# Kernel tuning notes

Measured on AMD Instinct MI355X. Metric: run time of the kernel, lower is better.

The kernel has to match this reference:

```python
import jax, jax.numpy as jnp
import numpy as np

LMAX, MMAX = 6, 2
CIN = COUT = 128
NUM_EDGES = 50000
NUM_M_COMP = (LMAX + 1) + sum(2 * (LMAX + 1 - m) for m in range(1, MMAX + 1))  # 29


def setup_inputs() -> dict:
    key = jax.random.key(0)
    ks = jax.random.split(key, 4)
    x = jax.random.normal(ks[0], (NUM_EDGES, NUM_M_COMP, CIN), dtype=jnp.float32)
    d0 = (LMAX + 1) * CIN  # 896
    W0 = jax.random.normal(ks[1], (d0, d0), dtype=jnp.float32) / np.float32(np.sqrt(d0))
    b0 = jnp.zeros((d0,), dtype=jnp.float32)
    Ws = []
    for i, m in enumerate(range(1, MMAX + 1)):
        din = (LMAX + 1 - m) * CIN
        dout = (LMAX + 1 - m) * COUT
        # torch Linear init then mul_(1/sqrt(2)); random scaled init suffices for a baseline
        Ws.append(jax.random.normal(ks[2 + i], (2 * dout, din), dtype=jnp.float32)
                  / np.float32(np.sqrt(2.0) * np.sqrt(din)))
    return {"x": x, "W0": W0, "b0": b0, "W1": Ws[0], "W2": Ws[1]}


def reference(x, W0, b0, W1, W2):
    E = x.shape[0]
    Wm = [W1, W2]
    outs = []
    # m = 0 block: flatten (lmax+1, Cin) -> single Linear with bias
    x0 = x[:, :LMAX + 1].reshape(E, (LMAX + 1) * CIN)
    y0 = x0 @ W0.T + b0                               # [E, (lmax+1)*Cout]
    outs.append(y0.reshape(E, LMAX + 1, COUT))
    offset = LMAX + 1
    for m in range(1, MMAX + 1):
        n = LMAX + 1 - m
        xm = x[:, offset:offset + 2 * n].reshape(E, 2, n * CIN)  # [E, 2(real/imag), n*Cin]
        offset += 2 * n
        ym = jnp.einsum('eti,oi->eto', xm, Wm[m - 1])            # [E, 2, 2*n*Cout]
        of = n * COUT
        x_r, x_i = ym[..., :of], ym[..., of:]
        pos = x_r[:, 0] - x_i[:, 1]                              # [E, n*Cout]
        neg = x_r[:, 1] + x_i[:, 0]
        outs.append(pos.reshape(E, n, COUT))
        outs.append(neg.reshape(E, n, COUT))
    return jnp.concatenate(outs, axis=1)  # [E, num_m_components, Cout]
```

## Files before the change

kernel.cpp:

```cpp
#include <hip/hip_runtime.h>
#include <hip/hip_bf16.h>
#include <cstdint>
#include <cstddef>

typedef __bf16 bf16_t;
typedef __bf16 bf16x8 __attribute__((ext_vector_type(8)));
typedef __bf16 bf16x4 __attribute__((ext_vector_type(4)));
typedef float f32x4 __attribute__((ext_vector_type(4)));

static constexpr int LD = 29 * 128;


__global__ void cvt_w0_pad_kernel(const float* __restrict__ in, bf16_t* __restrict__ out,
                                  int rows_real, int kdim, int total) {
    int idx = blockIdx.x * 256 + threadIdx.x;
    if (idx >= total) return;
    int r = idx / kdim;
    int c = idx - r * kdim;
    out[idx] = (bf16_t)((r < rows_real) ? in[(size_t)r * kdim + c] : 0.f);
}

__global__ void combine_wm_kernel(const float* __restrict__ W, bf16_t* __restrict__ Wc,
                                  int of, int din, int total) {
    int idx = blockIdx.x * 256 + threadIdx.x;
    if (idx >= total) return;
    int twodin = 2 * din;
    int r = idx / twodin;
    int c = idx - r * twodin;
    float v;
    if (r < of) {
        v = (c < din) ? W[(size_t)r * din + c]
                      : -W[(size_t)(r + of) * din + (c - din)];
    } else {
        int j = r - of;
        v = (c < din) ? W[(size_t)(j + of) * din + c]
                      : W[(size_t)j * din + (c - din)];
    }
    Wc[idx] = (bf16_t)v;
}

__global__ void cvt_x_kernel(const float* __restrict__ in, bf16_t* __restrict__ out, long n8) {
    long stride = (long)gridDim.x * 256;
    for (long i = blockIdx.x * 256L + threadIdx.x; i < n8; i += stride) {
        f32x4 v0 = *(const f32x4*)(in + i * 8);
        f32x4 v1 = *(const f32x4*)(in + i * 8 + 4);
        bf16x8 h;
        h[0] = (bf16_t)v0[0]; h[1] = (bf16_t)v0[1];
        h[2] = (bf16_t)v0[2]; h[3] = (bf16_t)v0[3];
        h[4] = (bf16_t)v1[0]; h[5] = (bf16_t)v1[1];
        h[6] = (bf16_t)v1[2]; h[7] = (bf16_t)v1[3];
        *(bf16x8*)(out + i * 8) = h;
    }
}


#define MMA_Q(QM, QN, AF)                                                            \
    do {                                                                             \
        __builtin_amdgcn_s_setprio(1);                                               \
        _Pragma("unroll") for (int i_ = 0; i_ < 2; ++i_)                             \
        _Pragma("unroll") for (int j_ = 0; j_ < 4; ++j_)                             \
        _Pragma("unroll") for (int kk_ = 0; kk_ < 2; ++kk_)                          \
            acc[QM][QN][i_][j_] = __builtin_amdgcn_mfma_f32_16x16x32_bf16(           \
                AF[i_][kk_], b[j_][kk_], acc[QM][QN][i_][j_], 0, 0, 0);              \
        __builtin_amdgcn_s_setprio(0);                                               \
    } while (0)

#define BAR() __builtin_amdgcn_s_barrier()
#define LGKM0()                                                   \
    do {                                                          \
        asm volatile("s_waitcnt lgkmcnt(0)" ::: "memory");        \
        __builtin_amdgcn_sched_barrier(0);                        \
    } while (0)

template <int NPAD, int K, int NREAL, bool BIAS>
__global__ __launch_bounds__(512, 2)
void gemm256_kernel(const bf16_t* __restrict__ Xb, const bf16_t* __restrict__ W,
                    const float* __restrict__ bias, float* __restrict__ Y, int M) {
    constexpr int NT  = K / 64;
    constexpr int NIT = NT / 2;
    static_assert(NT % 2 == 0, "NT must be even");

    __shared__ bf16_t lds[2][2][2][128][64];

    const int tid  = threadIdx.x;
    const int wid  = tid >> 6;
    const int lane = tid & 63;
    const int awr  = wid & 3;
    const int bwc  = wid >> 2;
    const int lrow = lane & 15;
    const int koff = lane >> 4;

    const long m0 = (long)blockIdx.y * 256;
    const long n0 = (long)blockIdx.x * 256;

    const int sr = tid >> 3;
    const int sc = tid & 7;

    auto stage_half = [&](int bu, int op, int half, int kt) {
        #pragma unroll
        for (int s = 0; s < 2; ++s) {
            const int r  = s * 64 + sr;
            const int kc = sc ^ (r & 7);
            long grow = (op ? n0 : m0) + half * 128 + r;
            if (!op && grow >= M) grow = M - 1;
            const bf16_t* gsrc = (op ? W : Xb) + grow * (op ? (long)K : (long)LD) + kt * 64 + kc * 8;
            bf16_t* dst = &lds[bu][op][half][0][0] + s * 4096 + wid * 512;
            __builtin_amdgcn_global_load_lds(
                (const __attribute__((address_space(1))) void*)gsrc,
                (__attribute__((address_space(3))) void*)dst, 16, 0, 0);
        }
    };

    bf16x8 a0[2][2], a1[2][2], b[4][2];
    f32x4 acc[2][2][2][4] = {};

    auto load_a = [&](bf16x8 (&a)[2][2], int bu, int half) {
        #pragma unroll
        for (int i = 0; i < 2; ++i)
            #pragma unroll
            for (int kk = 0; kk < 2; ++kk) {
                const int rr = awr * 32 + i * 16 + lrow;
                const int sw = (kk * 4 + koff) ^ (rr & 7);
                a[i][kk] = *(const bf16x8*)(&lds[bu][0][half][rr][sw * 8]);
            }
    };
    auto load_b = [&](int bu, int half) {
        #pragma unroll
        for (int j = 0; j < 4; ++j)
            #pragma unroll
            for (int kk = 0; kk < 2; ++kk) {
                const int rr = bwc * 64 + j * 16 + lrow;
                const int sw = (kk * 4 + koff) ^ (rr & 7);
                b[j][kk] = *(const bf16x8*)(&lds[bu][1][half][rr][sw * 8]);
            }
    };

    auto half_iter = [&](int bu, int ts, bool do_stage, bool lastvm) {
        load_a(a0, bu, 0);
        load_b(bu, 0);
        BAR(); LGKM0();
        MMA_Q(0, 0, a0);
        BAR();
        load_a(a1, bu, 1);
        if (do_stage) { stage_half(bu, 0, 0, ts); stage_half(bu, 1, 0, ts); }
        BAR(); LGKM0();
        MMA_Q(1, 0, a1);
        BAR();
        load_b(bu, 1);
        if (do_stage) stage_half(bu, 0, 1, ts);
        BAR(); LGKM0();
        MMA_Q(1, 1, a1);
        BAR();
        if (do_stage) stage_half(bu, 1, 1, ts);
        if (lastvm) asm volatile("s_waitcnt vmcnt(0)" ::: "memory");
        else        asm volatile("s_waitcnt vmcnt(8)" ::: "memory");
        BAR(); LGKM0();
        MMA_Q(0, 1, a0);
        BAR();
    };

    #pragma unroll
    for (int h = 0; h < 2; ++h) { stage_half(0, 0, h, 0); stage_half(0, 1, h, 0); }
    #pragma unroll
    for (int h = 0; h < 2; ++h) { stage_half(1, 0, h, 1); stage_half(1, 1, h, 1); }
    asm volatile("s_waitcnt vmcnt(8)" ::: "memory");
    BAR();

    #pragma unroll 1
    for (int it = 0; it < NIT; ++it) {
        const bool st = (it < NIT - 1);
        const bool lv = (it == NIT - 1);
        half_iter(0, 2 * it + 2, st, lv);
        half_iter(1, 2 * it + 3, st, lv);
    }

    #pragma unroll
    for (int qm = 0; qm < 2; ++qm)
        #pragma unroll
        for (int qn = 0; qn < 2; ++qn)
            #pragma unroll
            for (int j = 0; j < 4; ++j) {
                const long col = n0 + qn * 128 + bwc * 64 + j * 16 + lrow;
                if (col < NREAL) {
                    float bv = 0.f;
                    if constexpr (BIAS) bv = bias[col];
                    #pragma unroll
                    for (int i = 0; i < 2; ++i) {
                        const long rbase = m0 + qm * 128 + awr * 32 + i * 16 + koff * 4;
                        #pragma unroll
                        for (int r = 0; r < 4; ++r) {
                            const long row = rbase + r;
                            if (row < M) Y[row * LD + col] = acc[qm][qn][i][j][r] + bv;
                        }
                    }
                }
            }
}


template <int N, int K, bool BIAS>
__global__ __launch_bounds__(256)
void gemm_fb_kernel(const float* __restrict__ X, const bf16_t* __restrict__ W,
                    const float* __restrict__ bias, float* __restrict__ Y, int M) {
    constexpr int BM = 128, BK = 32;
    constexpr int KT = K / BK;
    __shared__ bf16_t As[BM][BK + 8];
    __shared__ bf16_t Bs[BM][BK];
    const int tid = threadIdx.x, wid = tid >> 6, lane = tid & 63;
    const int wr = wid >> 1, wc = wid & 1;
    const int m0 = blockIdx.y * BM, n0 = blockIdx.x * 128;
    const int srow0 = wid * 16 + (lane >> 2), schunk = lane & 3;
    const int ar = tid >> 3, ac = (tid & 7) * 4;
    const int lrow = lane & 15, koff = lane >> 4;
    f32x4 acc[4][4] = {};
    for (int kt = 0; kt < KT; ++kt) {
        const int k0 = kt * BK;
        #pragma unroll
        for (int s = 0; s < 2; ++s) {
            const int row = srow0 + s * 64;
            const int kc = schunk ^ ((row >> 1) & 3);
            const bf16_t* gsrc = W + (size_t)(n0 + row) * K + k0 + kc * 8;
            bf16_t* ldsbase = &Bs[wid * 16 + s * 64][0];
            __builtin_amdgcn_global_load_lds(
                (const __attribute__((address_space(1))) void*)gsrc,
                (__attribute__((address_space(3))) void*)ldsbase, 16, 0, 0);
        }
        #pragma unroll
        for (int p = 0; p < 4; ++p) {
            const int row = p * 32 + ar;
            const int gr = m0 + row;
            f32x4 v = {};
            if (gr < M) v = *(const f32x4*)(X + (size_t)gr * LD + k0 + ac);
            bf16x4 h;
            h[0] = (bf16_t)v[0]; h[1] = (bf16_t)v[1];
            h[2] = (bf16_t)v[2]; h[3] = (bf16_t)v[3];
            *(bf16x4*)(&As[row][ac]) = h;
        }
        __syncthreads();
        bf16x8 a[4], bb[4];
        #pragma unroll
        for (int i = 0; i < 4; ++i) {
            a[i] = *(const bf16x8*)(&As[wr * 64 + i * 16 + lrow][koff * 8]);
            const int col = wc * 64 + i * 16 + lrow;
            const int kc = koff ^ ((col >> 1) & 3);
            bb[i] = *(const bf16x8*)(&Bs[col][kc * 8]);
        }
        #pragma unroll
        for (int i = 0; i < 4; ++i)
            #pragma unroll
            for (int j = 0; j < 4; ++j)
                acc[i][j] = __builtin_amdgcn_mfma_f32_16x16x32_bf16(a[i], bb[j], acc[i][j], 0, 0, 0);
        __syncthreads();
    }
    #pragma unroll
    for (int j = 0; j < 4; ++j) {
        const int col = n0 + wc * 64 + j * 16 + lrow;
        float bv = 0.f;
        if constexpr (BIAS) bv = bias[col];
        #pragma unroll
        for (int i = 0; i < 4; ++i) {
            const int rbase = m0 + wr * 64 + i * 16 + koff * 4;
            #pragma unroll
            for (int r = 0; r < 4; ++r) {
                const int gr = rbase + r;
                if (gr < M) Y[(size_t)gr * LD + col] = acc[i][j][r] + bv;
            }
        }
    }
}


extern "C" void kernel_launch(void* const* d_in, const int* in_sizes, int n_in,
                              void* d_out, int out_size, void* d_ws, size_t ws_size,
                              hipStream_t stream) {
    const float* x  = (const float*)d_in[0];
    const float* W0 = (const float*)d_in[1];
    const float* b0 = (const float*)d_in[2];
    const float* W1 = (const float*)d_in[3];
    const float* W2 = (const float*)d_in[4];
    float* out = (float*)d_out;

    const int E = in_sizes[0] / LD;

    constexpr size_t W0P = (size_t)1024 * 896;
    constexpr size_t W1S = (size_t)1536 * 1536;
    constexpr size_t W2S = (size_t)1280 * 1280;
    bf16_t* wc0 = (bf16_t*)d_ws;
    bf16_t* wc1 = wc0 + W0P;
    bf16_t* wc2 = wc1 + W1S;
    bf16_t* xb  = wc2 + W2S;

    const size_t need = (W0P + W1S + W2S + (size_t)E * LD) * sizeof(bf16_t);
    const bool fast = ws_size >= need;

    cvt_w0_pad_kernel<<<(int)((W0P + 255) / 256), 256, 0, stream>>>(W0, wc0, 896, 896, (int)W0P);
    combine_wm_kernel<<<(int)(W1S / 256), 256, 0, stream>>>(W1, wc1, 768, 768, (int)W1S);
    combine_wm_kernel<<<(int)(W2S / 256), 256, 0, stream>>>(W2, wc2, 640, 640, (int)W2S);

    if (fast) {
        const long n8 = (long)E * LD / 8;
        cvt_x_kernel<<<4096, 256, 0, stream>>>(x, xb, n8);
        const int mt = (E + 255) / 256;
        gemm256_kernel<1024, 896, 896, true>
            <<<dim3(4, mt), 512, 0, stream>>>(xb, wc0, b0, out, E);
        gemm256_kernel<1536, 1536, 1536, false>
            <<<dim3(6, mt), 512, 0, stream>>>(xb + 896, wc1, nullptr, out + 896, E);
        gemm256_kernel<1280, 1280, 1280, false>
            <<<dim3(5, mt), 512, 0, stream>>>(xb + 2432, wc2, nullptr, out + 2432, E);
    } else {
        const int mt = (E + 127) / 128;
        gemm_fb_kernel<896, 896, true>
            <<<dim3(896 / 128, mt), 256, 0, stream>>>(x, wc0, b0, out, E);
        gemm_fb_kernel<1536, 1536, false>
            <<<dim3(1536 / 128, mt), 256, 0, stream>>>(x + 896, wc1, nullptr, out + 896, E);
        gemm_fb_kernel<1280, 1280, false>
            <<<dim3(1280 / 128, mt), 256, 0, stream>>>(x + 2432, wc2, nullptr, out + 2432, E);
    }
}
```

Measured before the change: 864.0 us.

## Merge three GEMMs into one persistent kernel with cross-tile prefetch

Replaces the three separate templated GEMM launches with a single persistent kernel of 256 blocks. Each block walks a flat tile list covering all three m-blocks, using a runtime tile descriptor. The first k-slices of the next tile are staged while the current tile finishes, so the pipeline does not drain between tiles. This removes launch gaps and per-launch tail effects. In exchange K and NT become runtime values (fewer compile-time constants), the epilogue uses a runtime bias check, and tiles with different K are mixed in one static round-robin schedule that may balance poorly.

```diff
diff --git a/kernel.cpp b/kernel.cpp
--- a/kernel.cpp
+++ b/kernel.cpp
@@ -54,6 +54,17 @@
 }
 
 
+struct TileDesc {
+    const bf16_t* A;
+    const bf16_t* W;
+    float* Y;
+    const float* bias;
+    long m0;
+    int K;
+    int NT;
+    int ncol;
+};
+
 #define MMA_Q(QM, QN, AF)                                                            \
     do {                                                                             \
         __builtin_amdgcn_s_setprio(1);                                               \
@@ -72,14 +83,14 @@
         __builtin_amdgcn_sched_barrier(0);                        \
     } while (0)
 
-template <int NPAD, int K, int NREAL, bool BIAS>
 __global__ __launch_bounds__(512, 2)
-void gemm256_kernel(const bf16_t* __restrict__ Xb, const bf16_t* __restrict__ W,
-                    const float* __restrict__ bias, float* __restrict__ Y, int M) {
-    constexpr int NT  = K / 64;
-    constexpr int NIT = NT / 2;
-    static_assert(NT % 2 == 0, "NT must be even");
-
+void gemm_persist_kernel(const bf16_t* __restrict__ xb,
+                         const bf16_t* __restrict__ w0,
+                         const bf16_t* __restrict__ w1,
+                         const bf16_t* __restrict__ w2,
+                         const float* __restrict__ b0,
+                         float* __restrict__ out,
+                         int E, int mt, int ntiles) {
     __shared__ bf16_t lds[2][2][2][128][64];
 
     const int tid  = threadIdx.x;
@@ -89,21 +100,49 @@
     const int bwc  = wid >> 2;
     const int lrow = lane & 15;
     const int koff = lane >> 4;
-
-    const long m0 = (long)blockIdx.y * 256;
-    const long n0 = (long)blockIdx.x * 256;
-
-    const int sr = tid >> 3;
-    const int sc = tid & 7;
-
-    auto stage_half = [&](int bu, int op, int half, int kt) {
+    const int sr   = tid >> 3;
+    const int sc   = tid & 7;
+    const int P    = gridDim.x;
+
+    int t = blockIdx.x;
+    if (t >= ntiles) return;
+
+    auto make_desc = [&](int tt, TileDesc& d) {
+        const int S0 = 4 * mt, S1 = S0 + 6 * mt;
+        int mi, ni;
+        if (tt < S0) {
+            mi = tt >> 2; ni = tt & 3;
+            d.A = xb; d.W = w0 + (size_t)ni * 256 * 896;
+            d.Y = out + ni * 256; d.bias = b0 + ni * 256;
+            d.K = 896; d.NT = 14;
+            d.ncol = (896 - ni * 256 < 256) ? (896 - ni * 256) : 256;
+        } else if (tt < S1) {
+            int l = tt - S0; mi = l / 6; ni = l - mi * 6;
+            d.A = xb + 896; d.W = w1 + (size_t)ni * 256 * 1536;
+            d.Y = out + 896 + ni * 256; d.bias = nullptr;
+            d.K = 1536; d.NT = 24; d.ncol = 256;
+        } else {
+            int l = tt - S1; mi = l / 5; ni = l - mi * 5;
+            d.A = xb + 2432; d.W = w2 + (size_t)ni * 256 * 1280;
+            d.Y = out + 2432 + ni * 256; d.bias = nullptr;
+            d.K = 1280; d.NT = 20; d.ncol = 256;
+        }
+        d.m0 = (long)mi * 256;
+    };
+
+    auto stage_half = [&](const TileDesc& d, int kt, int bu, int op, int half) {
         #pragma unroll
         for (int s = 0; s < 2; ++s) {
             const int r  = s * 64 + sr;
             const int kc = sc ^ (r & 7);
-            long grow = (op ? n0 : m0) + half * 128 + r;
-            if (!op && grow >= M) grow = M - 1;
-            const bf16_t* gsrc = (op ? W : Xb) + grow * (op ? (long)K : (long)LD) + kt * 64 + kc * 8;
+            const bf16_t* gsrc;
+            if (op) {
+                gsrc = d.W + (size_t)(half * 128 + r) * d.K + kt * 64 + kc * 8;
+            } else {
+                long grow = d.m0 + half * 128 + r;
+                if (grow >= E) grow = E - 1;
+                gsrc = d.A + grow * (long)LD + kt * 64 + kc * 8;
+            }
             bf16_t* dst = &lds[bu][op][half][0][0] + s * 4096 + wid * 512;
             __builtin_amdgcn_global_load_lds(
                 (const __attribute__((address_space(1))) void*)gsrc,
@@ -135,66 +174,102 @@
             }
     };
 
-    auto half_iter = [&](int bu, int ts, bool do_stage, bool lastvm) {
+    auto half_iter = [&](int bu, const TileDesc& sd, int skt, bool dostage) {
         load_a(a0, bu, 0);
         load_b(bu, 0);
         BAR(); LGKM0();
         MMA_Q(0, 0, a0);
         BAR();
         load_a(a1, bu, 1);
-        if (do_stage) { stage_half(bu, 0, 0, ts); stage_half(bu, 1, 0, ts); }
+        if (dostage) { stage_half(sd, skt, bu, 0, 0); stage_half(sd, skt, bu, 1, 0); }
         BAR(); LGKM0();
         MMA_Q(1, 0, a1);
         BAR();
         load_b(bu, 1);
-        if (do_stage) stage_half(bu, 0, 1, ts);
+        if (dostage) stage_half(sd, skt, bu, 0, 1);
         BAR(); LGKM0();
         MMA_Q(1, 1, a1);
         BAR();
-        if (do_stage) stage_half(bu, 1, 1, ts);
-        if (lastvm) asm volatile("s_waitcnt vmcnt(0)" ::: "memory");
-        else        asm volatile("s_waitcnt vmcnt(8)" ::: "memory");
+        if (dostage) {
+            stage_half(sd, skt, bu, 1, 1);
+            asm volatile("s_waitcnt vmcnt(8)" ::: "memory");
+        } else {
+            asm volatile("s_waitcnt vmcnt(0)" ::: "memory");
+        }
         BAR(); LGKM0();
         MMA_Q(0, 1, a0);
         BAR();
     };
 
-    #pragma unroll
-    for (int h = 0; h < 2; ++h) { stage_half(0, 0, h, 0); stage_half(0, 1, h, 0); }
-    #pragma unroll
-    for (int h = 0; h < 2; ++h) { stage_half(1, 0, h, 1); stage_half(1, 1, h, 1); }
-    asm volatile("s_waitcnt vmcnt(8)" ::: "memory");
-    BAR();
-
-    #pragma unroll 1
-    for (int it = 0; it < NIT; ++it) {
-        const bool st = (it < NIT - 1);
-        const bool lv = (it == NIT - 1);
-        half_iter(0, 2 * it + 2, st, lv);
-        half_iter(1, 2 * it + 3, st, lv);
-    }
-
-    #pragma unroll
-    for (int qm = 0; qm < 2; ++qm)
-        #pragma unroll
-        for (int qn = 0; qn < 2; ++qn)
-            #pragma unroll
-            for (int j = 0; j < 4; ++j) {
-                const long col = n0 + qn * 128 + bwc * 64 + j * 16 + lrow;
-                if (col < NREAL) {
-                    float bv = 0.f;
-                    if constexpr (BIAS) bv = bias[col];
-                    #pragma unroll
-                    for (int i = 0; i < 2; ++i) {
-                        const long rbase = m0 + qm * 128 + awr * 32 + i * 16 + koff * 4;
+    auto epilogue = [&](const TileDesc& d) {
+        #pragma unroll
+        for (int qm = 0; qm < 2; ++qm)
+            #pragma unroll
+            for (int qn = 0; qn < 2; ++qn)
+                #pragma unroll
+                for (int j = 0; j < 4; ++j) {
+                    const int col = qn * 128 + bwc * 64 + j * 16 + lrow;
+                    if (col < d.ncol) {
+                        const float bv = d.bias ? d.bias[col] : 0.f;
                         #pragma unroll
-                        for (int r = 0; r < 4; ++r) {
-                            const long row = rbase + r;
-                            if (row < M) Y[row * LD + col] = acc[qm][qn][i][j][r] + bv;
+                        for (int i = 0; i < 2; ++i) {
+                            const long rb = d.m0 + qm * 128 + awr * 32 + i * 16 + koff * 4;
+                            #pragma unroll
+                            for (int r = 0; r < 4; ++r) {
+                                const long row = rb + r;
+                                if (row < E) d.Y[row * LD + col] = acc[qm][qn][i][j][r] + bv;
+                            }
                         }
                     }
                 }
-            }
+    };
+
+    TileDesc cur, nxt;
+    make_desc(t, cur);
+    int tn = t + P;
+    bool has_nxt = tn < ntiles;
+    if (has_nxt) make_desc(tn, nxt);
+
+    stage_half(cur, 0, 0, 0, 0); stage_half(cur, 0, 0, 0, 1);
+    stage_half(cur, 0, 0, 1, 0); stage_half(cur, 0, 0, 1, 1);
+    stage_half(cur, 1, 1, 0, 0); stage_half(cur, 1, 1, 0, 1);
+    stage_half(cur, 1, 1, 1, 0); stage_half(cur, 1, 1, 1, 1);
+    asm volatile("s_waitcnt vmcnt(8)" ::: "memory");
+    BAR();
+
+    while (true) {
+        const int NITc = cur.NT >> 1;
+        #pragma unroll 1
+        for (int it = 0; it < NITc - 1; ++it) {
+            half_iter(0, cur, 2 * it + 2, true);
+            half_iter(1, cur, 2 * it + 3, true);
+        }
+        if (has_nxt) {
+            half_iter(0, nxt, 0, true);
+            half_iter(1, nxt, 1, true);
+        } else {
+            half_iter(0, cur, 0, false);
+            half_iter(1, cur, 0, false);
+        }
+
+        epilogue(cur);
+
+        if (!has_nxt) break;
+        cur = nxt;
+        t = tn; tn = t + P;
+        has_nxt = tn < ntiles;
+        if (has_nxt) make_desc(tn, nxt);
+
+        #pragma unroll
+        for (int qm = 0; qm < 2; ++qm)
+            #pragma unroll
+            for (int qn = 0; qn < 2; ++qn)
+                #pragma unroll
+                for (int i = 0; i < 2; ++i)
+                    #pragma unroll
+                    for (int j = 0; j < 4; ++j)
+                        acc[qm][qn][i][j] = (f32x4){0.f, 0.f, 0.f, 0.f};
+    }
 }
 
 
@@ -301,12 +376,8 @@
         const long n8 = (long)E * LD / 8;
         cvt_x_kernel<<<4096, 256, 0, stream>>>(x, xb, n8);
         const int mt = (E + 255) / 256;
-        gemm256_kernel<1024, 896, 896, true>
-            <<<dim3(4, mt), 512, 0, stream>>>(xb, wc0, b0, out, E);
-        gemm256_kernel<1536, 1536, 1536, false>
-            <<<dim3(6, mt), 512, 0, stream>>>(xb + 896, wc1, nullptr, out + 896, E);
-        gemm256_kernel<1280, 1280, 1280, false>
-            <<<dim3(5, mt), 512, 0, stream>>>(xb + 2432, wc2, nullptr, out + 2432, E);
+        const int ntiles = 15 * mt;
+        gemm_persist_kernel<<<dim3(256), 512, 0, stream>>>(xb, wc0, wc1, wc2, b0, out, E, mt, ntiles);
     } else {
         const int mt = (E + 127) / 128;
         gemm_fb_kernel<896, 896, true>
```

Result: slower. 1.437 ms (+66.3%).

## Merge three per-m GEMM launches into one grouped kernel with block remapping

Applied to the files above, without the earlier changes.

Replaces the three separate gemm256 launches with a single grouped kernel whose 1D grid covers the tiles of all three GEMMs. Each block dispatches to a templated tile body by segment. A seg_remap swizzle groups blocks so that 8 M-tiles sharing a weight column tile run close together, which should improve L2 reuse. This removes the tail and launch gaps between kernels, at the cost of a branchy kernel whose segments have different K lengths. It also peels the last pipeline iteration out of the main loop.

```diff
diff --git a/kernel.cpp b/kernel.cpp
--- a/kernel.cpp
+++ b/kernel.cpp
@@ -72,15 +72,17 @@
         __builtin_amdgcn_sched_barrier(0);                        \
     } while (0)
 
-template <int NPAD, int K, int NREAL, bool BIAS>
-__global__ __launch_bounds__(512, 2)
-void gemm256_kernel(const bf16_t* __restrict__ Xb, const bf16_t* __restrict__ W,
-                    const float* __restrict__ bias, float* __restrict__ Y, int M) {
-    constexpr int NT  = K / 64;
+typedef bf16_t lds_t[2][2][2][128][64];
+
+template <int K, int NT, bool BIAS>
+__device__ __forceinline__ void gemm_tile_body(
+        const bf16_t* __restrict__ A,
+        const bf16_t* __restrict__ Wn,
+        const float* __restrict__ biasn,
+        float* __restrict__ Yn,
+        long m0, int ncol, int E, lds_t& lds) {
     constexpr int NIT = NT / 2;
-    static_assert(NT % 2 == 0, "NT must be even");
-
-    __shared__ bf16_t lds[2][2][2][128][64];
+    static_assert(NT % 2 == 0, "NT even");
 
     const int tid  = threadIdx.x;
     const int wid  = tid >> 6;
@@ -89,21 +91,22 @@
     const int bwc  = wid >> 2;
     const int lrow = lane & 15;
     const int koff = lane >> 4;
-
-    const long m0 = (long)blockIdx.y * 256;
-    const long n0 = (long)blockIdx.x * 256;
-
-    const int sr = tid >> 3;
-    const int sc = tid & 7;
-
-    auto stage_half = [&](int bu, int op, int half, int kt) {
+    const int sr   = tid >> 3;
+    const int sc   = tid & 7;
+
+    auto stage_half = [&](int kt, int bu, int op, int half) {
         #pragma unroll
         for (int s = 0; s < 2; ++s) {
             const int r  = s * 64 + sr;
             const int kc = sc ^ (r & 7);
-            long grow = (op ? n0 : m0) + half * 128 + r;
-            if (!op && grow >= M) grow = M - 1;
-            const bf16_t* gsrc = (op ? W : Xb) + grow * (op ? (long)K : (long)LD) + kt * 64 + kc * 8;
+            const bf16_t* gsrc;
+            if (op) {
+                gsrc = Wn + (size_t)(half * 128 + r) * K + kt * 64 + kc * 8;
+            } else {
+                long grow = m0 + half * 128 + r;
+                if (grow >= E) grow = E - 1;
+                gsrc = A + grow * (long)LD + kt * 64 + kc * 8;
+            }
             bf16_t* dst = &lds[bu][op][half][0][0] + s * 4096 + wid * 512;
             __builtin_amdgcn_global_load_lds(
                 (const __attribute__((address_space(1))) void*)gsrc,
@@ -135,44 +138,47 @@
             }
     };
 
-    auto half_iter = [&](int bu, int ts, bool do_stage, bool lastvm) {
+    auto half_iter = [&](int bu, int skt, bool dostage) {
         load_a(a0, bu, 0);
         load_b(bu, 0);
         BAR(); LGKM0();
         MMA_Q(0, 0, a0);
         BAR();
         load_a(a1, bu, 1);
-        if (do_stage) { stage_half(bu, 0, 0, ts); stage_half(bu, 1, 0, ts); }
+        if (dostage) { stage_half(skt, bu, 0, 0); stage_half(skt, bu, 1, 0); }
         BAR(); LGKM0();
         MMA_Q(1, 0, a1);
         BAR();
         load_b(bu, 1);
-        if (do_stage) stage_half(bu, 0, 1, ts);
+        if (dostage) stage_half(skt, bu, 0, 1);
         BAR(); LGKM0();
         MMA_Q(1, 1, a1);
         BAR();
-        if (do_stage) stage_half(bu, 1, 1, ts);
-        if (lastvm) asm volatile("s_waitcnt vmcnt(0)" ::: "memory");
-        else        asm volatile("s_waitcnt vmcnt(8)" ::: "memory");
+        if (dostage) {
+            stage_half(skt, bu, 1, 1);
+            asm volatile("s_waitcnt vmcnt(8)" ::: "memory");
+        } else {
+            asm volatile("s_waitcnt vmcnt(0)" ::: "memory");
+        }
         BAR(); LGKM0();
         MMA_Q(0, 1, a0);
         BAR();
     };
 
-    #pragma unroll
-    for (int h = 0; h < 2; ++h) { stage_half(0, 0, h, 0); stage_half(0, 1, h, 0); }
-    #pragma unroll
-    for (int h = 0; h < 2; ++h) { stage_half(1, 0, h, 1); stage_half(1, 1, h, 1); }
+    stage_half(0, 0, 0, 0); stage_half(0, 0, 0, 1);
+    stage_half(0, 0, 1, 0); stage_half(0, 0, 1, 1);
+    stage_half(1, 1, 0, 0); stage_half(1, 1, 0, 1);
+    stage_half(1, 1, 1, 0); stage_half(1, 1, 1, 1);
     asm volatile("s_waitcnt vmcnt(8)" ::: "memory");
     BAR();
 
     #pragma unroll 1
-    for (int it = 0; it < NIT; ++it) {
-        const bool st = (it < NIT - 1);
-        const bool lv = (it == NIT - 1);
-        half_iter(0, 2 * it + 2, st, lv);
-        half_iter(1, 2 * it + 3, st, lv);
-    }
+    for (int it = 0; it < NIT - 1; ++it) {
+        half_iter(0, 2 * it + 2, true);
+        half_iter(1, 2 * it + 3, true);
+    }
+    half_iter(0, 0, false);
+    half_iter(1, 0, false);
 
     #pragma unroll
     for (int qm = 0; qm < 2; ++qm)
@@ -180,21 +186,67 @@
         for (int qn = 0; qn < 2; ++qn)
             #pragma unroll
             for (int j = 0; j < 4; ++j) {
-                const long col = n0 + qn * 128 + bwc * 64 + j * 16 + lrow;
-                if (col < NREAL) {
+                const int col = qn * 128 + bwc * 64 + j * 16 + lrow;
+                if (col < ncol) {
                     float bv = 0.f;
-                    if constexpr (BIAS) bv = bias[col];
+                    if constexpr (BIAS) bv = biasn[col];
                     #pragma unroll
                     for (int i = 0; i < 2; ++i) {
-                        const long rbase = m0 + qm * 128 + awr * 32 + i * 16 + koff * 4;
+                        const long rb = m0 + qm * 128 + awr * 32 + i * 16 + koff * 4;
                         #pragma unroll
                         for (int r = 0; r < 4; ++r) {
-                            const long row = rbase + r;
-                            if (row < M) Y[row * LD + col] = acc[qm][qn][i][j][r] + bv;
+                            const long row = rb + r;
+                            if (row < E) Yn[row * LD + col] = acc[qm][qn][i][j][r] + bv;
                         }
                     }
                 }
             }
+}
+
+__device__ __forceinline__ int seg_remap(int lb, int ncol, int mt) {
+    const int g8   = (mt >> 3) << 3;
+    const int full = g8 * ncol;
+    if (lb < full) {
+        const int x  = lb & 7;
+        const int s  = lb >> 3;
+        const int s4 = s / ncol;
+        const int mem = s - s4 * ncol;
+        return (s4 * 8 + x) * ncol + mem;
+    }
+    return lb;
+}
+
+__global__ __launch_bounds__(512, 2)
+void gemm_all_kernel(const bf16_t* __restrict__ xb,
+                     const bf16_t* __restrict__ w0,
+                     const bf16_t* __restrict__ w1,
+                     const bf16_t* __restrict__ w2,
+                     const float* __restrict__ b0,
+                     float* __restrict__ out,
+                     int E, int mt) {
+    __shared__ lds_t lds;
+
+    const int b  = blockIdx.x;
+    const int S0 = 4 * mt;
+    const int S1 = S0 + 6 * mt;
+
+    if (b < S0) {
+        const int lt = seg_remap(b, 4, mt);
+        const int mi = lt >> 2, ni = lt & 3;
+        const int ncol = (ni == 3) ? 128 : 256;
+        gemm_tile_body<896, 14, true>(xb, w0 + (size_t)ni * 256 * 896, b0 + ni * 256,
+                                      out + ni * 256, (long)mi * 256, ncol, E, lds);
+    } else if (b < S1) {
+        const int lt = seg_remap(b - S0, 6, mt);
+        const int mi = lt / 6, ni = lt - mi * 6;
+        gemm_tile_body<1536, 24, false>(xb + 896, w1 + (size_t)ni * 256 * 1536, nullptr,
+                                        out + 896 + ni * 256, (long)mi * 256, 256, E, lds);
+    } else {
+        const int lt = seg_remap(b - S1, 5, mt);
+        const int mi = lt / 5, ni = lt - mi * 5;
+        gemm_tile_body<1280, 20, false>(xb + 2432, w2 + (size_t)ni * 256 * 1280, nullptr,
+                                        out + 2432 + ni * 256, (long)mi * 256, 256, E, lds);
+    }
 }
 
 
@@ -301,12 +353,7 @@
         const long n8 = (long)E * LD / 8;
         cvt_x_kernel<<<4096, 256, 0, stream>>>(x, xb, n8);
         const int mt = (E + 255) / 256;
-        gemm256_kernel<1024, 896, 896, true>
-            <<<dim3(4, mt), 512, 0, stream>>>(xb, wc0, b0, out, E);
-        gemm256_kernel<1536, 1536, 1536, false>
-            <<<dim3(6, mt), 512, 0, stream>>>(xb + 896, wc1, nullptr, out + 896, E);
-        gemm256_kernel<1280, 1280, 1280, false>
-            <<<dim3(5, mt), 512, 0, stream>>>(xb + 2432, wc2, nullptr, out + 2432, E);
+        gemm_all_kernel<<<dim3(15 * mt), 512, 0, stream>>>(xb, wc0, wc1, wc2, b0, out, E, mt);
     } else {
         const int mt = (E + 127) / 128;
         gemm_fb_kernel<896, 896, true>
```

Result: faster. 813.5 us (-5.8%).
